# Optimization experiments

Measured on AMD Instinct MI355X. Metric: run time of the kernel, lower is better.

Reference implementation:

```python
import jax, jax.numpy as jnp
import numpy as np


def setup_inputs() -> dict:
    key = jax.random.key(0)
    k1, k2, k3 = jax.random.split(key, 3)
    B, T, D, U = 64, 1024, 256, 512
    inputs = jax.random.normal(k1, (B, T, D), dtype=jnp.float32)
    W_xh = jax.random.normal(k2, (D, U), dtype=jnp.float32) * (1.0 / np.sqrt(D))
    W_hh = jax.random.normal(k3, (U, U), dtype=jnp.float32) * (1.0 / np.sqrt(U))
    b_h = jnp.zeros((U,), dtype=jnp.float32)
    return {"inputs": inputs, "W_xh": W_xh, "W_hh": W_hh, "b_h": b_h}


def reference(inputs, W_xh, W_hh, b_h):
    # h_t = tanh(x_t @ W_xh + h_{t-1} @ W_hh + b_h); return_sequences=True
    B, T, D = inputs.shape
    U = W_hh.shape[0]
    # input projection is time-independent: precompute once (same math)
    xw = jnp.einsum('btd,du->btu', inputs, W_xh) + b_h  # (B, T, U)
    h0 = jnp.zeros((B, U), dtype=inputs.dtype)

    def step(h_prev, xw_t):
        h_t = jnp.tanh(xw_t + h_prev @ W_hh)
        return h_t, h_t

    _, hs = jax.lax.scan(step, h0, jnp.swapaxes(xw, 0, 1))  # (T, B, U)
    return jnp.swapaxes(hs, 0, 1)  # (B, T, U)
```

## Files before the change

kernel.cpp:

```cpp
#include <hip/hip_runtime.h>


typedef __attribute__((ext_vector_type(8))) short short8;
typedef __attribute__((ext_vector_type(4))) float f32x4;

#define T_SZ 1024
#define U_SZ 512

typedef union { unsigned long long q[2]; short8 v; } chunk16;

__device__ __forceinline__ unsigned short f2bf(float f){
  unsigned u = __float_as_uint(f);
  u += 0x7FFFu + ((u >> 16) & 1u);
  return (unsigned short)(u >> 16);
}
__device__ __forceinline__ float bf2f(unsigned short s){
  return __uint_as_float(((unsigned)s) << 16);
}

__global__ __launch_bounds__(256) void xw_gemm(const float* __restrict__ X,
                                               const float* __restrict__ W,
                                               const float* __restrict__ bias,
                                               float* __restrict__ out){
  __shared__ float As[16][132];
  __shared__ float Bs[16][68];
  const int tid = threadIdx.x;
  const int tx = tid & 15, ty = tid >> 4;
  const int row0 = blockIdx.x * 128;
  const int col0 = blockIdx.y * 64;
  float acc[8][4];
  #pragma unroll
  for(int a=0;a<8;a++)
    #pragma unroll
    for(int b=0;b<4;b++) acc[a][b]=0.f;

  for(int kc=0;kc<256;kc+=16){
    {
      const int m  = tid >> 2;
      const int kq = (tid & 3) * 4;
      #pragma unroll
      for(int h=0;h<2;h++){
        const float4 v = *(const float4*)&X[(size_t)(row0 + m + 64*h)*256 + kc + kq];
        As[kq+0][m+64*h]=v.x; As[kq+1][m+64*h]=v.y;
        As[kq+2][m+64*h]=v.z; As[kq+3][m+64*h]=v.w;
      }
    }
    {
      const int k = tid >> 4;
      const int c = (tid & 15) * 4;
      *(float4*)&Bs[k][c] = *(const float4*)&W[(size_t)(kc + k)*512 + col0 + c];
    }
    __syncthreads();
    #pragma unroll
    for(int k=0;k<16;k++){
      const float4 b4 = *(const float4*)&Bs[k][tx*4];
      const float4 a0 = *(const float4*)&As[k][ty*8];
      const float4 a1 = *(const float4*)&As[k][ty*8+4];
      const float av[8] = {a0.x,a0.y,a0.z,a0.w,a1.x,a1.y,a1.z,a1.w};
      const float bv[4] = {b4.x,b4.y,b4.z,b4.w};
      #pragma unroll
      for(int ii=0;ii<8;ii++)
        #pragma unroll
        for(int j=0;j<4;j++) acc[ii][j] = fmaf(av[ii], bv[j], acc[ii][j]);
    }
    __syncthreads();
  }
  #pragma unroll
  for(int ii=0;ii<8;ii++){
    const int row = row0 + ty*8 + ii;
    float4 o;
    o.x = acc[ii][0] + bias[col0+tx*4+0];
    o.y = acc[ii][1] + bias[col0+tx*4+1];
    o.z = acc[ii][2] + bias[col0+tx*4+2];
    o.w = acc[ii][3] + bias[col0+tx*4+3];
    *(float4*)&out[(size_t)row*512 + col0 + tx*4] = o;
  }
}

__global__ __launch_bounds__(256, 1) void rnn_rec(const float* __restrict__ Whh,
                                                  float* __restrict__ out,
                                                  int* __restrict__ flags,
                                                  unsigned short* __restrict__ ring){
  __shared__ unsigned short Ahi[16][520];
  __shared__ unsigned short Alo[16][520];
  __shared__ float red[2][64][4];

  const int bid = blockIdx.x;
  const int g  = bid & 3;
  const int i  = bid >> 2;
  const int tid = threadIdx.x;
  const int lane = tid & 63;
  const int w  = tid >> 6;
  const int nt = w & 1;
  const int kh = w >> 1;
  const int ln = lane & 15;
  const int lq = lane >> 4;
  const int b0 = g * 16;
  const int c0 = i * 32;
  const int ncol0 = c0 + nt * 16;

  short8 whi[8], wlo[8];
  #pragma unroll
  for(int kt=0;kt<8;kt++){
    short8 h8, l8;
    const int kb = kh*256 + kt*32 + lq*8;
    #pragma unroll
    for(int j=0;j<8;j++){
      const float wv = Whh[(size_t)(kb+j)*512 + ncol0 + ln];
      const unsigned short hb = f2bf(wv);
      const unsigned short lb = f2bf(wv - bf2f(hb));
      h8[j] = (short)hb; l8[j] = (short)lb;
    }
    whi[kt]=h8; wlo[kt]=l8;
  }
  for(int idx=tid; idx<16*520; idx+=256){
    ((unsigned short*)Ahi)[idx]=0;
    ((unsigned short*)Alo)[idx]=0;
  }
  __syncthreads();

  float xwv[4] = {0.f,0.f,0.f,0.f};
  float hprev[4] = {0.f,0.f,0.f,0.f};
  if(kh==0){
    #pragma unroll
    for(int r=0;r<4;r++)
      xwv[r] = out[((size_t)(b0 + lq*4 + r)*T_SZ + 0)*U_SZ + ncol0 + ln];
  }

  for(int t=0;t<T_SZ;t++){
    if(t>0){
      if(kh==0){
        #pragma unroll
        for(int r=0;r<4;r++)
          out[((size_t)(b0 + lq*4 + r)*T_SZ + (t-1))*U_SZ + ncol0 + ln] = hprev[r];
      }
      {
        const int s2 = lane >> 1;
        const int ntf = lane & 1;
        const int p = w + 4*s2;
        bool done = (lane>=8) || (p==i);
        while(__ballot(!done)){
          if(!done){
            const int f = __hip_atomic_load(&flags[((g*16+p)<<1)|ntf],
                                            __ATOMIC_RELAXED, __HIP_MEMORY_SCOPE_AGENT);
            done = (f >= t);
          }
        }
      }
      asm volatile("" ::: "memory");
      const size_t slot = (size_t)((t-1)&1);
      #pragma unroll
      for(int s3=0;s3<4;s3++){
        const int p = w + 4*s3;
        if(p==i) continue;
        const unsigned long long* rb =
            (const unsigned long long*)ring + ((slot*4 + g)*16 + p)*256;
        chunk16 ch, cl;
        ch.q[0] = __hip_atomic_load(rb + (size_t)lane*2 + 0,   __ATOMIC_RELAXED, __HIP_MEMORY_SCOPE_AGENT);
        ch.q[1] = __hip_atomic_load(rb + (size_t)lane*2 + 1,   __ATOMIC_RELAXED, __HIP_MEMORY_SCOPE_AGENT);
        cl.q[0] = __hip_atomic_load(rb + 128 + (size_t)lane*2, __ATOMIC_RELAXED, __HIP_MEMORY_SCOPE_AGENT);
        cl.q[1] = __hip_atomic_load(rb + 129 + (size_t)lane*2, __ATOMIC_RELAXED, __HIP_MEMORY_SCOPE_AGENT);
        const int kd = p*32 + lq*8;
        *(short8*)&Ahi[ln][kd] = ch.v;
        *(short8*)&Alo[ln][kd] = cl.v;
      }
    }
    __syncthreads();

    f32x4 c_hh = {0.f,0.f,0.f,0.f}, c_hl = {0.f,0.f,0.f,0.f}, c_lh = {0.f,0.f,0.f,0.f};
    #pragma unroll
    for(int kt=0;kt<8;kt++){
      const int k = kh*256 + kt*32 + lq*8;
      const short8 ah = *(const short8*)&Ahi[ln][k];
      const short8 al = *(const short8*)&Alo[ln][k];
      c_hh = __builtin_amdgcn_mfma_f32_16x16x32_bf16(ah, whi[kt], c_hh, 0, 0, 0);
      c_hl = __builtin_amdgcn_mfma_f32_16x16x32_bf16(ah, wlo[kt], c_hl, 0, 0, 0);
      c_lh = __builtin_amdgcn_mfma_f32_16x16x32_bf16(al, whi[kt], c_lh, 0, 0, 0);
    }
    f32x4 csum = c_hh + c_hl + c_lh;
    if(kh==1) *(f32x4*)&red[nt][lane][0] = csum;
    __syncthreads();
    if(kh==0){
      const f32x4 o = *(const f32x4*)&red[nt][lane][0];
      csum += o;
      #pragma unroll
      for(int r=0;r<4;r++){
        float pre = csum[r] + xwv[r];
        pre = fminf(fmaxf(pre, -12.f), 12.f);
        const float e = __expf(2.f*pre);
        const float h = (e-1.f)/(e+1.f);
        hprev[r] = h;
        const unsigned short hb = f2bf(h);
        const unsigned short lb = f2bf(h - bf2f(hb));
        Ahi[lq*4+r][ncol0+ln] = hb;
        Alo[lq*4+r][ncol0+ln] = lb;
      }
      {
        const int c  = lane & 31;
        const int m  = c >> 1;
        const int q  = nt*2 + (c & 1);
        const int sel = lane >> 5;
        const unsigned short* src = sel ? &Alo[m][c0 + q*8] : &Ahi[m][c0 + q*8];
        chunk16 ck; ck.v = *(const short8*)src;
        unsigned long long* rb = (unsigned long long*)ring
            + (((size_t)(t&1)*4 + g)*16 + i)*256 + (size_t)sel*128 + (size_t)(q*16 + m)*2;
        __hip_atomic_store(rb+0, ck.q[0], __ATOMIC_RELAXED, __HIP_MEMORY_SCOPE_AGENT);
        __hip_atomic_store(rb+1, ck.q[1], __ATOMIC_RELAXED, __HIP_MEMORY_SCOPE_AGENT);
      }
      asm volatile("s_waitcnt vmcnt(0)" ::: "memory");
      if(lane==0)
        __hip_atomic_store(&flags[((g*16+i)<<1)|nt], t+1,
                           __ATOMIC_RELAXED, __HIP_MEMORY_SCOPE_AGENT);
      {
        const int tn = (t < T_SZ-1) ? t+1 : t;
        #pragma unroll
        for(int r=0;r<4;r++)
          xwv[r] = out[((size_t)(b0 + lq*4 + r)*T_SZ + tn)*U_SZ + ncol0 + ln];
      }
    }
  }
  if(kh==0){
    #pragma unroll
    for(int r=0;r<4;r++)
      out[((size_t)(b0 + lq*4 + r)*T_SZ + (T_SZ-1))*U_SZ + ncol0 + ln] = hprev[r];
  }
}

extern "C" void kernel_launch(void* const* d_in, const int* in_sizes, int n_in,
                              void* d_out, int out_size, void* d_ws, size_t ws_size,
                              hipStream_t stream) {
  (void)in_sizes; (void)n_in; (void)out_size; (void)ws_size;
  const float* X   = (const float*)d_in[0];
  const float* Wxh = (const float*)d_in[1];
  const float* Whh = (const float*)d_in[2];
  const float* bh  = (const float*)d_in[3];
  float* out = (float*)d_out;

  int* flags = (int*)d_ws;
  unsigned short* ring = (unsigned short*)((char*)d_ws + 1024);

  xw_gemm<<<dim3(512, 8), 256, 0, stream>>>(X, Wxh, bh, out);
  rnn_rec<<<64, 256, 0, stream>>>(Whh, out, flags, ring);
}
```

Baseline: 3.671 ms.

## Repartition recurrence across 16 larger blocks with full-K per wave and double-buffered LDS

Reworks the recurrent kernel from 64 blocks of 256 threads to 16 blocks of 512 threads. Each block now owns 128 output columns, and each wave computes the full K=512 reduction, which removes the cross-wave LDS reduction and its extra barrier. The h-state LDS buffers are double-buffered so each step needs only one __syncthreads. Each block now polls and exchanges with 3 peers instead of 15, and flags are padded to separate cache lines. The cost is more weight registers per wave (16 hi/lo fragment pairs) and a longer serial MFMA chain per step.

```diff
diff --git a/kernel.cpp b/kernel.cpp
--- a/kernel.cpp
+++ b/kernel.cpp
@@ -77,13 +77,12 @@
   }
 }
 
-__global__ __launch_bounds__(256, 1) void rnn_rec(const float* __restrict__ Whh,
+__global__ __launch_bounds__(512, 2) void rnn_rec(const float* __restrict__ Whh,
                                                   float* __restrict__ out,
                                                   int* __restrict__ flags,
                                                   unsigned short* __restrict__ ring){
-  __shared__ unsigned short Ahi[16][520];
-  __shared__ unsigned short Alo[16][520];
-  __shared__ float red[2][64][4];
+  __shared__ unsigned short Ahi[2][16][520];
+  __shared__ unsigned short Alo[2][16][520];
 
   const int bid = blockIdx.x;
   const int g  = bid & 3;
@@ -91,57 +90,54 @@
   const int tid = threadIdx.x;
   const int lane = tid & 63;
   const int w  = tid >> 6;
-  const int nt = w & 1;
-  const int kh = w >> 1;
   const int ln = lane & 15;
   const int lq = lane >> 4;
   const int b0 = g * 16;
-  const int c0 = i * 32;
-  const int ncol0 = c0 + nt * 16;
-
-  short8 whi[8], wlo[8];
-  #pragma unroll
-  for(int kt=0;kt<8;kt++){
+  const int ncol0 = i*128 + w*16;
+
+  short8 whi[16], wlo[16];
+  #pragma unroll
+  for(int kt=0;kt<16;kt++){
     short8 h8, l8;
-    const int kb = kh*256 + kt*32 + lq*8;
+    const int kb = kt*32 + lq*8;
     #pragma unroll
     for(int j=0;j<8;j++){
-      const float wv = Whh[(size_t)(kb+j)*512 + ncol0 + ln];
+      const float wv = Whh[(size_t)(kb+j)*U_SZ + ncol0 + ln];
       const unsigned short hb = f2bf(wv);
       const unsigned short lb = f2bf(wv - bf2f(hb));
       h8[j] = (short)hb; l8[j] = (short)lb;
     }
     whi[kt]=h8; wlo[kt]=l8;
   }
-  for(int idx=tid; idx<16*520; idx+=256){
+  for(int idx=tid; idx<2*16*520; idx+=512){
     ((unsigned short*)Ahi)[idx]=0;
     ((unsigned short*)Alo)[idx]=0;
   }
   __syncthreads();
 
-  float xwv[4] = {0.f,0.f,0.f,0.f};
-  float hprev[4] = {0.f,0.f,0.f,0.f};
-  if(kh==0){
-    #pragma unroll
-    for(int r=0;r<4;r++)
-      xwv[r] = out[((size_t)(b0 + lq*4 + r)*T_SZ + 0)*U_SZ + ncol0 + ln];
-  }
+  float xwv[4], hprev[4];
+  #pragma unroll
+  for(int r=0;r<4;r++){
+    xwv[r] = out[((size_t)(b0 + lq*4 + r)*T_SZ + 0)*U_SZ + ncol0 + ln];
+    hprev[r] = 0.f;
+  }
+
+  const int selp = lane >> 5;
+  const int mrow = (lane & 31) >> 1;
+  const int qh   = lane & 1;
 
   for(int t=0;t<T_SZ;t++){
+    const int buf = t & 1;
     if(t>0){
-      if(kh==0){
-        #pragma unroll
-        for(int r=0;r<4;r++)
-          out[((size_t)(b0 + lq*4 + r)*T_SZ + (t-1))*U_SZ + ncol0 + ln] = hprev[r];
-      }
+      #pragma unroll
+      for(int r=0;r<4;r++)
+        out[((size_t)(b0 + lq*4 + r)*T_SZ + (t-1))*U_SZ + ncol0 + ln] = hprev[r];
       {
-        const int s2 = lane >> 1;
-        const int ntf = lane & 1;
-        const int p = w + 4*s2;
-        bool done = (lane>=8) || (p==i);
+        const int p = lane + (lane >= i);
+        bool done = (lane >= 3);
         while(__ballot(!done)){
           if(!done){
-            const int f = __hip_atomic_load(&flags[((g*16+p)<<1)|ntf],
+            const int f = __hip_atomic_load(&flags[((g*4+p)*8 + w)*32],
                                             __ATOMIC_RELAXED, __HIP_MEMORY_SCOPE_AGENT);
             done = (f >= t);
           }
@@ -150,80 +146,67 @@
       asm volatile("" ::: "memory");
       const size_t slot = (size_t)((t-1)&1);
       #pragma unroll
-      for(int s3=0;s3<4;s3++){
-        const int p = w + 4*s3;
-        if(p==i) continue;
-        const unsigned long long* rb =
-            (const unsigned long long*)ring + ((slot*4 + g)*16 + p)*256;
-        chunk16 ch, cl;
-        ch.q[0] = __hip_atomic_load(rb + (size_t)lane*2 + 0,   __ATOMIC_RELAXED, __HIP_MEMORY_SCOPE_AGENT);
-        ch.q[1] = __hip_atomic_load(rb + (size_t)lane*2 + 1,   __ATOMIC_RELAXED, __HIP_MEMORY_SCOPE_AGENT);
-        cl.q[0] = __hip_atomic_load(rb + 128 + (size_t)lane*2, __ATOMIC_RELAXED, __HIP_MEMORY_SCOPE_AGENT);
-        cl.q[1] = __hip_atomic_load(rb + 129 + (size_t)lane*2, __ATOMIC_RELAXED, __HIP_MEMORY_SCOPE_AGENT);
-        const int kd = p*32 + lq*8;
-        *(short8*)&Ahi[ln][kd] = ch.v;
-        *(short8*)&Alo[ln][kd] = cl.v;
+      for(int s=0;s<3;s++){
+        const int p = s + (s >= i);
+        const unsigned long long* rb = (const unsigned long long*)ring
+            + (((slot*4 + g)*4 + p)*8 + w)*128 + selp*64 + mrow*4 + qh*2;
+        chunk16 cc;
+        cc.q[0] = __hip_atomic_load(rb+0, __ATOMIC_RELAXED, __HIP_MEMORY_SCOPE_AGENT);
+        cc.q[1] = __hip_atomic_load(rb+1, __ATOMIC_RELAXED, __HIP_MEMORY_SCOPE_AGENT);
+        unsigned short* dst = selp ? &Alo[buf][mrow][p*128 + w*16 + qh*8]
+                                   : &Ahi[buf][mrow][p*128 + w*16 + qh*8];
+        *(short8*)dst = cc.v;
       }
     }
     __syncthreads();
 
     f32x4 c_hh = {0.f,0.f,0.f,0.f}, c_hl = {0.f,0.f,0.f,0.f}, c_lh = {0.f,0.f,0.f,0.f};
     #pragma unroll
-    for(int kt=0;kt<8;kt++){
-      const int k = kh*256 + kt*32 + lq*8;
-      const short8 ah = *(const short8*)&Ahi[ln][k];
-      const short8 al = *(const short8*)&Alo[ln][k];
+    for(int kt=0;kt<16;kt++){
+      const int k = kt*32 + lq*8;
+      const short8 ah = *(const short8*)&Ahi[buf][ln][k];
+      const short8 al = *(const short8*)&Alo[buf][ln][k];
       c_hh = __builtin_amdgcn_mfma_f32_16x16x32_bf16(ah, whi[kt], c_hh, 0, 0, 0);
       c_hl = __builtin_amdgcn_mfma_f32_16x16x32_bf16(ah, wlo[kt], c_hl, 0, 0, 0);
       c_lh = __builtin_amdgcn_mfma_f32_16x16x32_bf16(al, whi[kt], c_lh, 0, 0, 0);
     }
-    f32x4 csum = c_hh + c_hl + c_lh;
-    if(kh==1) *(f32x4*)&red[nt][lane][0] = csum;
-    __syncthreads();
-    if(kh==0){
-      const f32x4 o = *(const f32x4*)&red[nt][lane][0];
-      csum += o;
-      #pragma unroll
-      for(int r=0;r<4;r++){
-        float pre = csum[r] + xwv[r];
-        pre = fminf(fmaxf(pre, -12.f), 12.f);
-        const float e = __expf(2.f*pre);
-        const float h = (e-1.f)/(e+1.f);
-        hprev[r] = h;
-        const unsigned short hb = f2bf(h);
-        const unsigned short lb = f2bf(h - bf2f(hb));
-        Ahi[lq*4+r][ncol0+ln] = hb;
-        Alo[lq*4+r][ncol0+ln] = lb;
-      }
-      {
-        const int c  = lane & 31;
-        const int m  = c >> 1;
-        const int q  = nt*2 + (c & 1);
-        const int sel = lane >> 5;
-        const unsigned short* src = sel ? &Alo[m][c0 + q*8] : &Ahi[m][c0 + q*8];
-        chunk16 ck; ck.v = *(const short8*)src;
-        unsigned long long* rb = (unsigned long long*)ring
-            + (((size_t)(t&1)*4 + g)*16 + i)*256 + (size_t)sel*128 + (size_t)(q*16 + m)*2;
-        __hip_atomic_store(rb+0, ck.q[0], __ATOMIC_RELAXED, __HIP_MEMORY_SCOPE_AGENT);
-        __hip_atomic_store(rb+1, ck.q[1], __ATOMIC_RELAXED, __HIP_MEMORY_SCOPE_AGENT);
-      }
-      asm volatile("s_waitcnt vmcnt(0)" ::: "memory");
-      if(lane==0)
-        __hip_atomic_store(&flags[((g*16+i)<<1)|nt], t+1,
-                           __ATOMIC_RELAXED, __HIP_MEMORY_SCOPE_AGENT);
-      {
-        const int tn = (t < T_SZ-1) ? t+1 : t;
-        #pragma unroll
-        for(int r=0;r<4;r++)
-          xwv[r] = out[((size_t)(b0 + lq*4 + r)*T_SZ + tn)*U_SZ + ncol0 + ln];
-      }
-    }
-  }
-  if(kh==0){
-    #pragma unroll
-    for(int r=0;r<4;r++)
-      out[((size_t)(b0 + lq*4 + r)*T_SZ + (T_SZ-1))*U_SZ + ncol0 + ln] = hprev[r];
-  }
+    const f32x4 csum = c_hh + c_hl + c_lh;
+    const int nbuf = buf ^ 1;
+    #pragma unroll
+    for(int r=0;r<4;r++){
+      float pre = csum[r] + xwv[r];
+      pre = fminf(fmaxf(pre, -12.f), 12.f);
+      const float e = __expf(2.f*pre);
+      const float h = (e-1.f)/(e+1.f);
+      hprev[r] = h;
+      const unsigned short hb = f2bf(h);
+      const unsigned short lb = f2bf(h - bf2f(hb));
+      Ahi[nbuf][lq*4+r][ncol0+ln] = hb;
+      Alo[nbuf][lq*4+r][ncol0+ln] = lb;
+    }
+    {
+      const unsigned short* src = selp ? &Alo[nbuf][mrow][ncol0 + qh*8]
+                                       : &Ahi[nbuf][mrow][ncol0 + qh*8];
+      chunk16 ck; ck.v = *(const short8*)src;
+      unsigned long long* rb = (unsigned long long*)ring
+          + ((((size_t)(t&1)*4 + g)*4 + i)*8 + w)*128 + selp*64 + mrow*4 + qh*2;
+      __hip_atomic_store(rb+0, ck.q[0], __ATOMIC_RELAXED, __HIP_MEMORY_SCOPE_AGENT);
+      __hip_atomic_store(rb+1, ck.q[1], __ATOMIC_RELAXED, __HIP_MEMORY_SCOPE_AGENT);
+    }
+    asm volatile("s_waitcnt vmcnt(0)" ::: "memory");
+    if(lane==0)
+      __hip_atomic_store(&flags[((g*4+i)*8 + w)*32], t+1,
+                         __ATOMIC_RELAXED, __HIP_MEMORY_SCOPE_AGENT);
+    {
+      const int tn = (t < T_SZ-1) ? t+1 : t;
+      #pragma unroll
+      for(int r=0;r<4;r++)
+        xwv[r] = out[((size_t)(b0 + lq*4 + r)*T_SZ + tn)*U_SZ + ncol0 + ln];
+    }
+  }
+  #pragma unroll
+  for(int r=0;r<4;r++)
+    out[((size_t)(b0 + lq*4 + r)*T_SZ + (T_SZ-1))*U_SZ + ncol0 + ln] = hprev[r];
 }
 
 extern "C" void kernel_launch(void* const* d_in, const int* in_sizes, int n_in,
@@ -237,8 +220,8 @@
   float* out = (float*)d_out;
 
   int* flags = (int*)d_ws;
-  unsigned short* ring = (unsigned short*)((char*)d_ws + 1024);
+  unsigned short* ring = (unsigned short*)((char*)d_ws + 16384);
 
   xw_gemm<<<dim3(512, 8), 256, 0, stream>>>(X, Wxh, bh, out);
-  rnn_rec<<<64, 256, 0, stream>>>(Whh, out, flags, ring);
-}
+  rnn_rec<<<16, 512, 0, stream>>>(Whh, out, flags, ring);
+}
```

Result: no change. 3.674 ms (+0.1%).
